# Kernel tuning notes

Hardware: AMD Instinct MI355X
Metric: run time of the kernel (lower is better)

## Reference

```python
import jax, jax.numpy as jnp
import numpy as np
jax.config.update("jax_enable_x64", True)

SR = 44100
STATE_SIZE = 4096
RG0, R10, C10, C20 = 1.0e6, 4.7e5, 3.3e-9, 1.0e-9

# Reconstructed DK-method incidence matrices (3 circuit nodes, 1 vsrc):
#   Vin at node1; C1 node1->node2; R1 node2->gnd; pot top node2->node3;
#   pot bottom node3->gnd; C2 node3->gnd; output at node3 (pot wiper).
_Nu = np.array([[1., 0., 0.]])
_Nx = np.array([[1., -1., 0.], [0., 0., 1.]])
_Nr = np.array([[0., 1., 0.]])
_Nv = np.array([[0., 1., -1.], [0., 0., 1.]])
_No = np.array([[0., 0., 1.]])


def _preamp_forward(x, cond, state, alpha_rg, alpha_r1, alpha_c1, alpha_c2, cond_w, cond_b):
    f64 = jnp.float64
    T = 1.0 / SR
    Nu, Nx, Nr, Nv, No = (jnp.asarray(m, f64) for m in (_Nu, _Nx, _Nr, _Nv, _No))
    Zm = jnp.eye(2, dtype=f64)
    n_nodes, n_vsrc = 3, 1
    zpad = jnp.zeros((2, n_vsrc), f64)
    Nvp = jnp.concatenate([Nv, zpad], axis=1)                      # [2,4]
    Nxp = jnp.concatenate([Nx, zpad], axis=1)                      # [2,4]
    Nop = jnp.concatenate([No, jnp.zeros((1, n_vsrc), f64)], 1)    # [1,4]
    Nup = jnp.concatenate([jnp.zeros((n_nodes, n_vsrc), f64), jnp.eye(n_vsrc, dtype=f64)], 0)  # [4,1]

    # component updates (sigmoid-trimmed around nominal values)
    RG = (0.9 + jax.nn.sigmoid(alpha_rg[0]).astype(f64) * 0.2) * RG0
    R1 = (0.99 + jax.nn.sigmoid(alpha_r1[0]).astype(f64) * 0.02) * R10
    C1 = (0.9 + jax.nn.sigmoid(alpha_c1[0]).astype(f64) * 0.2) * C10
    C2 = (0.9 + jax.nn.sigmoid(alpha_c2[0]).astype(f64) * 0.2) * C20
    Gr = jnp.reshape(1.0 / R1, (1, 1))
    Gx = jnp.diag(jnp.stack([2.0 * C1 / T, 2.0 * C2 / T]))

    # cond block: affine -> sigmoid -> log pot taper
    pot = jax.nn.sigmoid(cond[:, 0] * cond_w[0] + cond_b[0])
    p = jnp.clip((jnp.power(10.0, pot) - 1.0) / 9.0, 1e-4, 1.0 - 1e-4).astype(f64)  # [B]

    # state-space update
    top = jnp.concatenate([Nr.T @ Gr @ Nr + Nx.T @ Gx @ Nx, Nu.T], axis=1)
    bot = jnp.concatenate([Nu, jnp.zeros((n_vsrc, n_vsrc), f64)], axis=1)
    So_inv = jnp.linalg.inv(jnp.concatenate([top, bot], axis=0))   # [4,4]
    Q = Nvp @ So_inv @ Nvp.T                                        # [2,2]
    Ux = Nxp @ So_inv @ Nvp.T                                       # [2,2]
    Uo = Nop @ So_inv @ Nvp.T                                       # [1,2]
    Uu = Nup.T @ So_inv @ Nvp.T                                     # [1,2]
    ZGx = 2.0 * Zm @ Gx
    Ao = ZGx @ Nxp @ So_inv @ Nxp.T - Zm
    Bo = ZGx @ Nxp @ So_inv @ Nup
    Do = Nop @ So_inv @ Nxp.T
    Eo = Nop @ So_inv @ Nup

    d = jnp.stack([(1.0 - p) * RG, p * RG], axis=-1)                # [B,2]
    Rv = d[:, :, None] * jnp.eye(2, dtype=f64)                      # [B,2,2] diag
    RvQ = jnp.linalg.inv(Rv + Q)                                    # [B,2,2]

    ZGxUx = ZGx @ Ux
    A = Ao - ZGxUx @ RvQ @ Ux.T                                     # [B,2,2]
    Bm = Bo - ZGxUx @ RvQ @ Uu.T                                    # [B,2,1]
    Dm = Do - Uo @ RvQ @ Ux.T                                       # [B,1,2]
    Em = Eo - Uo @ RvQ @ Uu.T                                       # [B,1,1]

    # quadratic characteristic poly [1, -tr, det] (= real part of prod(z-eig))
    def poly2(M):
        tr = M[..., 0, 0] + M[..., 1, 1]
        det = M[..., 0, 0] * M[..., 1, 1] - M[..., 0, 1] * M[..., 1, 0]
        return jnp.stack([jnp.ones_like(tr), -tr, det], axis=-1)    # [B,3]

    den = poly2(A)
    num = poly2(A - Bm @ Dm) + (Em[:, 0] - 1.0) * den

    nb = 1 + STATE_SIZE // 2
    z = jnp.exp(-1j * jnp.linspace(0.0, jnp.pi, nb))                # complex128 [nb]

    def polyval(c):  # Horner, highest degree first
        c = c.astype(jnp.complex128)
        return (c[:, 0, None] * z + c[:, 1, None]) * z + c[:, 2, None]  # [B,nb]

    h = polyval(num) / polyval(den)                                 # [B,nb]

    L = x.shape[1]
    st = jnp.concatenate([state[:, L:, :], x], axis=1).astype(f64)  # [B,S,1]
    sf = jnp.fft.rfft(st, axis=1)                                   # [B,nb,1]
    out = jnp.fft.irfft(sf * h[:, :, None], axis=1).astype(jnp.float32)
    return out[:, -L:, :]


def setup_inputs() -> dict:
    key = jax.random.key(0)
    k0, k1, k2 = jax.random.split(key, 3)
    B, L = 2048, 2048
    return {
        "x": jax.random.normal(k0, (B, L, 1), dtype=jnp.float32),
        "cond": jax.random.uniform(k1, (B, 1), dtype=jnp.float32),
        "state": jax.random.normal(k2, (B, STATE_SIZE, 1), dtype=jnp.float32) * 0.1,
        "alpha_rg": jnp.zeros((1,), jnp.float32),
        "alpha_r1": jnp.zeros((1,), jnp.float32),
        "alpha_c1": jnp.zeros((1,), jnp.float32),
        "alpha_c2": jnp.zeros((1,), jnp.float32),
        "cond_w": jnp.ones((1,), jnp.float32),
        "cond_b": jnp.zeros((1,), jnp.float32),
    }


def reference(x, cond, state, alpha_rg, alpha_r1, alpha_c1, alpha_c2, cond_w, cond_b):
    return _preamp_forward(x, cond, state, alpha_rg, alpha_r1, alpha_c1, alpha_c2, cond_w, cond_b)
```

## Files before the change

### kernel.cpp

```cpp
#include <hip/hip_runtime.h>
#include <math.h>

#define NFFT 4096
#define HALF 2048
#define LSEG 2048
#define SSZ 4096

typedef float v2f __attribute__((ext_vector_type(2)));
typedef float v4f __attribute__((ext_vector_type(4)));

static __device__ __forceinline__ v2f cmul(v2f a, v2f b) {
    v2f r;
    asm("v_pk_mul_f32 %0, %1, %2 op_sel:[0,0] op_sel_hi:[0,1]\n\t"
        "v_pk_fma_f32 %0, %1, %2, %0 op_sel:[1,1,0] op_sel_hi:[1,0,1] neg_lo:[1,0,0]"
        : "=&v"(r) : "v"(a), "v"(b));
    return r;
}

static __device__ __forceinline__ v2f cadd_mi(v2f c, v2f d) {
    v2f r;
    asm("v_pk_add_f32 %0, %1, %2 op_sel:[0,1] op_sel_hi:[1,0] neg_hi:[0,1]"
        : "=v"(r) : "v"(c), "v"(d));
    return r;
}

static __device__ __forceinline__ v2f cadd_pi(v2f c, v2f d) {
    v2f r;
    asm("v_pk_add_f32 %0, %1, %2 op_sel:[0,1] op_sel_hi:[1,0] neg_lo:[0,1]"
        : "=v"(r) : "v"(c), "v"(d));
    return r;
}

static __device__ __forceinline__ int PAD(int i) { return i + (i >> 4); }

template <int SGN>
static __device__ __forceinline__ void dft16(v2f r[16]) {
    v2f t[16];
#pragma unroll
    for (int n1 = 0; n1 < 4; ++n1) {
        v2f a = r[n1], b = r[n1 + 4], c = r[n1 + 8], d = r[n1 + 12];
        v2f A = a + c, B = b + d, C = a - c, D = b - d;
        t[n1 * 4 + 0] = A + B;
        t[n1 * 4 + 2] = A - B;
        if (SGN < 0) {
            t[n1 * 4 + 1] = cadd_mi(C, D);
            t[n1 * 4 + 3] = cadd_pi(C, D);
        } else {
            t[n1 * 4 + 1] = cadd_pi(C, D);
            t[n1 * 4 + 3] = cadd_mi(C, D);
        }
    }
    const float CC[10] = {1.f, 0.92387953251f, 0.70710678119f, 0.38268343236f, 0.f,
                          -0.38268343236f, -0.70710678119f, -0.92387953251f, -1.f, -0.92387953251f};
    const float SS[10] = {0.f, 0.38268343236f, 0.70710678119f, 0.92387953251f, 1.f,
                          0.92387953251f, 0.70710678119f, 0.38268343236f, 0.f, -0.38268343236f};
    const float S = (float)SGN;
#pragma unroll
    for (int n1 = 1; n1 < 4; ++n1) {
#pragma unroll
        for (int m2 = 1; m2 < 4; ++m2) {
            const int k = n1 * m2;
            t[n1 * 4 + m2] = cmul(t[n1 * 4 + m2], (v2f){CC[k], S * SS[k]});
        }
    }
#pragma unroll
    for (int m2 = 0; m2 < 4; ++m2) {
        v2f a = t[m2], b = t[4 + m2], c = t[8 + m2], d = t[12 + m2];
        v2f A = a + c, B = b + d, C = a - c, D = b - d;
        r[m2]     = A + B;
        r[m2 + 8] = A - B;
        if (SGN < 0) {
            r[m2 + 4]  = cadd_mi(C, D);
            r[m2 + 12] = cadd_pi(C, D);
        } else {
            r[m2 + 4]  = cadd_pi(C, D);
            r[m2 + 12] = cadd_mi(C, D);
        }
    }
}

static __device__ __forceinline__ void twiddle_chain(v2f r[16], v2f w1) {
    v2f w2 = cmul(w1, w1);
    v2f w3 = cmul(w2, w1);
    v2f w4 = cmul(w2, w2);
    v2f w5 = cmul(w4, w1);
    v2f w6 = cmul(w4, w2);
    v2f w7 = cmul(w4, w3);
    v2f w8 = cmul(w4, w4);
    r[1] = cmul(r[1], w1);   r[2] = cmul(r[2], w2);
    r[3] = cmul(r[3], w3);   r[4] = cmul(r[4], w4);
    r[5] = cmul(r[5], w5);   r[6] = cmul(r[6], w6);
    r[7] = cmul(r[7], w7);   r[8] = cmul(r[8], w8);
    r[9]  = cmul(r[9],  cmul(w8, w1));
    r[10] = cmul(r[10], cmul(w8, w2));
    r[11] = cmul(r[11], cmul(w8, w3));
    r[12] = cmul(r[12], cmul(w8, w4));
    r[13] = cmul(r[13], cmul(w8, w5));
    r[14] = cmul(r[14], cmul(w8, w6));
    r[15] = cmul(r[15], cmul(w8, w7));
}

__global__ __launch_bounds__(256, 4)
void preamp_fft_kernel(const float* __restrict__ x,
                       const float* __restrict__ state,
                       const float* __restrict__ cond,
                       const float* __restrict__ a_rg,
                       const float* __restrict__ a_r1,
                       const float* __restrict__ a_c1,
                       const float* __restrict__ a_c2,
                       const float* __restrict__ cond_w,
                       const float* __restrict__ cond_b,
                       float* __restrict__ out, int B) {
    __shared__ v2f a_s[NFFT + NFFT / 16];
    __shared__ float cf[10];

    const int t = threadIdx.x;
    const int b0 = 2 * blockIdx.x;
    const int b1 = (b0 + 1 < B) ? b0 + 1 : b0;

    const float* st0 = state + (size_t)b0 * SSZ + (SSZ - LSEG);
    const float* xb0 = x + (size_t)b0 * LSEG;
    const float* st1 = state + (size_t)b1 * SSZ + (SSZ - LSEG);
    const float* xb1 = x + (size_t)b1 * LSEG;

#pragma unroll
    for (int q = 0; q < 4; ++q) {
        const int i0 = (t + 256 * q) << 2;
        v4f fa, fb;
        if (q < 2) {
            fa = *(const v4f*)(st0 + i0);
            fb = *(const v4f*)(st1 + i0);
        } else {
            fa = *(const v4f*)(xb0 + (i0 - LSEG));
            fb = *(const v4f*)(xb1 + (i0 - LSEG));
        }
        const int p = PAD(i0);
        a_s[p + 0] = (v2f){fa.x, fb.x};
        a_s[p + 1] = (v2f){fa.y, fb.y};
        a_s[p + 2] = (v2f){fa.z, fb.z};
        a_s[p + 3] = (v2f){fa.w, fb.w};
    }

    if ((t & 127) == 0) {
        const int who = t >> 7;
        const int bb = who ? b1 : b0;

        const double RG = (0.9 + (double)(1.0f / (1.0f + expf(-a_rg[0]))) * 0.2) * 1.0e6;
        const double R1 = (0.99 + (double)(1.0f / (1.0f + expf(-a_r1[0]))) * 0.02) * 4.7e5;
        const double C1 = (0.9 + (double)(1.0f / (1.0f + expf(-a_c1[0]))) * 0.2) * 3.3e-9;
        const double C2 = (0.9 + (double)(1.0f / (1.0f + expf(-a_c2[0]))) * 0.2) * 1.0e-9;
        const double g1 = 1.0 / R1;
        const double gc1 = 2.0 * C1 * 44100.0;
        const double gc2 = 2.0 * C2 * 44100.0;

        float zf = cond[bb] * cond_w[0] + cond_b[0];
        float pot = 1.0f / (1.0f + expf(-zf));
        float prf = (powf(10.0f, pot) - 1.0f) / 9.0f;
        prf = fminf(fmaxf(prf, 1e-4f), 1.0f - 1e-4f);
        const double p = (double)prf;

        const double ds = gc1 + g1;
        double S[4][4] = {
            {0.0, 0.0,        0.0,       1.0},
            {0.0, 1.0 / ds,   0.0,       gc1 / ds},
            {0.0, 0.0,        1.0 / gc2, 0.0},
            {1.0, gc1 / ds,   0.0,       -gc1 * g1 / ds}};

        double Q00 = S[1][1] - S[1][2] - S[2][1] + S[2][2];
        double Q01 = S[1][2] - S[2][2];
        double Q10 = S[2][1] - S[2][2];
        double Q11 = S[2][2];

        double Ux00 = S[0][1] - S[0][2] - S[1][1] + S[1][2];
        double Ux01 = S[0][2] - S[1][2];
        double Ux10 = S[2][1] - S[2][2];
        double Ux11 = S[2][2];

        double Uo0 = S[2][1] - S[2][2], Uo1 = S[2][2];
        double Uu0 = S[3][1] - S[3][2], Uu1 = S[3][2];

        double P00 = S[0][0] - S[0][1] - S[1][0] + S[1][1];
        double P01 = S[0][2] - S[1][2];
        double P10 = S[2][0] - S[2][1];
        double P11 = S[2][2];

        double Ao00 = 2.0 * gc1 * P00 - 1.0, Ao01 = 2.0 * gc1 * P01;
        double Ao10 = 2.0 * gc2 * P10,       Ao11 = 2.0 * gc2 * P11 - 1.0;

        double Bo0 = 2.0 * gc1 * (S[0][3] - S[1][3]);
        double Bo1 = 2.0 * gc2 * S[2][3];

        double Do0 = S[2][0] - S[2][1], Do1 = S[2][2];
        double Eo  = S[2][3];

        double T00 = 2.0 * gc1 * Ux00, T01 = 2.0 * gc1 * Ux01;
        double T10 = 2.0 * gc2 * Ux10, T11 = 2.0 * gc2 * Ux11;

        double d0 = (1.0 - p) * RG, d1v = p * RG;
        double M00 = d0 + Q00, M01 = Q01, M10 = Q10, M11 = d1v + Q11;
        double idet = 1.0 / (M00 * M11 - M01 * M10);
        double G00 =  M11 * idet, G01 = -M01 * idet;
        double G10 = -M10 * idet, G11 =  M00 * idet;

        double TG00 = T00 * G00 + T01 * G10, TG01 = T00 * G01 + T01 * G11;
        double TG10 = T10 * G00 + T11 * G10, TG11 = T10 * G01 + T11 * G11;

        double A00 = Ao00 - (TG00 * Ux00 + TG01 * Ux01);
        double A01 = Ao01 - (TG00 * Ux10 + TG01 * Ux11);
        double A10 = Ao10 - (TG10 * Ux00 + TG11 * Ux01);
        double A11 = Ao11 - (TG10 * Ux10 + TG11 * Ux11);

        double Bm0 = Bo0 - (TG00 * Uu0 + TG01 * Uu1);
        double Bm1 = Bo1 - (TG10 * Uu0 + TG11 * Uu1);

        double w0v = Uo0 * G00 + Uo1 * G10, w1v = Uo0 * G01 + Uo1 * G11;
        double Dm0 = Do0 - (w0v * Ux00 + w1v * Ux01);
        double Dm1 = Do1 - (w0v * Ux10 + w1v * Ux11);
        double Em  = Eo  - (w0v * Uu0 + w1v * Uu1);

        double den1 = -(A00 + A11);
        double den2 = A00 * A11 - A01 * A10;
        double Mm00 = A00 - Bm0 * Dm0, Mm01 = A01 - Bm0 * Dm1;
        double Mm10 = A10 - Bm1 * Dm0, Mm11 = A11 - Bm1 * Dm1;
        double num0 = Em;
        double num1 = -(Mm00 + Mm11) + (Em - 1.0) * den1;
        double num2 = (Mm00 * Mm11 - Mm01 * Mm10) + (Em - 1.0) * den2;

        cf[who * 5 + 0] = (float)num0;
        cf[who * 5 + 1] = (float)num1;
        cf[who * 5 + 2] = (float)(num0 + num1 + num2);
        cf[who * 5 + 3] = (float)den1;
        cf[who * 5 + 4] = (float)(1.0 + den1 + den2);
    }
    __syncthreads();

    const float TW4096 = 0.00153398078788564f;
    const float TW256  = 0.02454369260617026f;
    const float HW4096 = 0.00076699039394282f;

    float swA, cwA;
    __sincosf((float)t * TW4096, &swA, &cwA);
    const int subB = t >> 4, jB = t & 15;
    float swB, cwB;
    __sincosf((float)jB * TW256, &swB, &cwB);

    v2f r[16];

#pragma unroll
    for (int m = 0; m < 16; ++m) r[m] = a_s[PAD(t + 256 * m)];
    dft16<-1>(r);
    twiddle_chain(r, (v2f){cwA, -swA});
#pragma unroll
    for (int m = 0; m < 16; ++m) a_s[PAD(t + 256 * m)] = r[m];
    __syncthreads();

    {
        const int base = subB * 256 + jB;
#pragma unroll
        for (int m = 0; m < 16; ++m) r[m] = a_s[PAD(base + 16 * m)];
        dft16<-1>(r);
        twiddle_chain(r, (v2f){cwB, -swB});
#pragma unroll
        for (int m = 0; m < 16; ++m) a_s[PAD(base + 16 * m)] = r[m];
    }
    __syncthreads();

    {
        const int base = 16 * t;
#pragma unroll
        for (int m = 0; m < 16; ++m) r[m] = a_s[PAD(base + m)];
        dft16<-1>(r);
        const int klo = ((t & 15) << 4) | (t >> 4);
        __syncthreads();
#pragma unroll
        for (int m = 0; m < 16; ++m) a_s[PAD((m << 8) | klo)] = r[m];
    }
    __syncthreads();

    {
        const v2f n0p = {0.5f * cf[0], 0.5f * cf[5]};
        const v2f n1p = {0.5f * cf[1], 0.5f * cf[6]};
        const v2f snp = {0.5f * cf[2], 0.5f * cf[7]};
        const v2f d1p = {cf[3], cf[8]};
        const v2f sdp = {cf[4], cf[9]};

        for (int j = 0; j < 8; ++j) {
            const int k  = t + 256 * j;
            const int kr = (NFFT - k) & (NFFT - 1);
            v2f Wk = a_s[PAD(k)];
            v2f Wr = a_s[PAD(kr)];
            float Xar = Wk.x + Wr.x, Xai = Wk.y - Wr.y;
            float Xbr = Wk.y + Wr.y, Xbi = Wr.x - Wk.x;
            float sh, ch;
            __sincosf((float)k * HW4096, &sh, &ch);
            float m2s = -2.0f * sh;
            float ur = m2s * sh, ui = m2s * ch, pr = ur + 2.0f;
            v2f urp = {ur, ur}, uip = {ui, ui}, prp = {pr, pr};

            v2f tr = n0p * prp + n1p;
            v2f ti = n0p * uip;
            v2f nr = snp + urp * tr - uip * ti;
            v2f ni = urp * ti + uip * tr;
            v2f tb = prp + d1p;
            v2f dr = sdp + urp * tb - uip * uip;
            v2f di = urp * uip + uip * tb;
            v2f mg = dr * dr + di * di;
            v2f iv = { __builtin_amdgcn_rcpf(mg.x), __builtin_amdgcn_rcpf(mg.y) };
            v2f Hr = (nr * dr + ni * di) * iv;
            v2f Hi = (ni * dr - nr * di) * iv;

            float Yar = Hr.x * Xar - Hi.x * Xai, Yai = Hr.x * Xai + Hi.x * Xar;
            float Ybr = Hr.y * Xbr - Hi.y * Xbi, Ybi = Hr.y * Xbi + Hi.y * Xbr;
            a_s[PAD(k)]  = (v2f){Yar - Ybi, Yai + Ybr};
            a_s[PAD(kr)] = (v2f){Yar + Ybi, Ybr - Yai};
        }
        if (t == 0) {
            v2f Wn = a_s[PAD(2048)];
            float Ha = (snp.x - 2.0f * n1p.x) / (sdp.x - 2.0f * d1p.x);
            float Hb = (snp.y - 2.0f * n1p.y) / (sdp.y - 2.0f * d1p.y);
            a_s[PAD(2048)] = (v2f){Ha * (2.0f * Wn.x), Hb * (2.0f * Wn.y)};
        }
    }
    __syncthreads();

    {
        const int base = 16 * t;
        const int klo = ((t & 15) << 4) | (t >> 4);
#pragma unroll
        for (int m = 0; m < 16; ++m) r[m] = a_s[PAD((m << 8) | klo)];
        dft16<1>(r);
        __syncthreads();
#pragma unroll
        for (int m = 0; m < 16; ++m) a_s[PAD(base + m)] = r[m];
    }
    __syncthreads();

    {
        const int base = subB * 256 + jB;
#pragma unroll
        for (int m = 0; m < 16; ++m) r[m] = a_s[PAD(base + 16 * m)];
        twiddle_chain(r, (v2f){cwB, swB});
        dft16<1>(r);
#pragma unroll
        for (int m = 0; m < 16; ++m) a_s[PAD(base + 16 * m)] = r[m];
    }
    __syncthreads();

    {
#pragma unroll
        for (int m = 0; m < 16; ++m) r[m] = a_s[PAD(t + 256 * m)];
        twiddle_chain(r, (v2f){cwA, swA});
        dft16<1>(r);
        const float scale = 1.0f / (float)NFFT;
        float* ob0 = out + (size_t)b0 * LSEG;
        float* ob1 = out + (size_t)b1 * LSEG;
#pragma unroll
        for (int m = 8; m < 16; ++m) {
            const int idx = t + 256 * (m - 8);
            float ya = r[m].x * scale;
            float yb = (b1 != b0) ? r[m].y * scale : ya;
            ob0[idx] = ya;
            ob1[idx] = yb;
        }
    }
}

extern "C" void kernel_launch(void* const* d_in, const int* in_sizes, int n_in,
                              void* d_out, int out_size, void* d_ws, size_t ws_size,
                              hipStream_t stream) {
    const float* x     = (const float*)d_in[0];
    const float* cond  = (const float*)d_in[1];
    const float* state = (const float*)d_in[2];
    const float* a_rg  = (const float*)d_in[3];
    const float* a_r1  = (const float*)d_in[4];
    const float* a_c1  = (const float*)d_in[5];
    const float* a_c2  = (const float*)d_in[6];
    const float* c_w   = (const float*)d_in[7];
    const float* c_b   = (const float*)d_in[8];
    float* out = (float*)d_out;

    const int B = in_sizes[1];

    preamp_fft_kernel<<<dim3((B + 1) / 2), dim3(256), 0, stream>>>(
        x, state, cond, a_rg, a_r1, a_c1, a_c2, c_w, c_b, out, B);
}
```

Measured before the change: 113.0 us.

## Switch FFT to radix-8 with 512 threads and split coefficient computation into prepass

Rewrites the 4096-point FFT from three radix-16 passes over 256 threads to four radix-8 passes over 512 threads, which lowers register pressure per thread and raises the thread count per block. The per-batch double-precision filter coefficient computation moves out of the FFT kernel into a separate small kernel that writes to workspace, so the FFT kernel no longer stalls on one serial thread. The cost is an extra launch, a global round-trip for the coefficients, and more shared-memory passes and barriers.

```diff
diff --git a/kernel.cpp b/kernel.cpp
--- a/kernel.cpp
+++ b/kernel.cpp
@@ -16,14 +16,12 @@
         : "=&v"(r) : "v"(a), "v"(b));
     return r;
 }
-
 static __device__ __forceinline__ v2f cadd_mi(v2f c, v2f d) {
     v2f r;
     asm("v_pk_add_f32 %0, %1, %2 op_sel:[0,1] op_sel_hi:[1,0] neg_hi:[0,1]"
         : "=v"(r) : "v"(c), "v"(d));
     return r;
 }
-
 static __device__ __forceinline__ v2f cadd_pi(v2f c, v2f d) {
     v2f r;
     asm("v_pk_add_f32 %0, %1, %2 op_sel:[0,1] op_sel_hi:[1,0] neg_lo:[0,1]"
@@ -34,85 +32,147 @@
 static __device__ __forceinline__ int PAD(int i) { return i + (i >> 4); }
 
 template <int SGN>
-static __device__ __forceinline__ void dft16(v2f r[16]) {
-    v2f t[16];
-#pragma unroll
-    for (int n1 = 0; n1 < 4; ++n1) {
-        v2f a = r[n1], b = r[n1 + 4], c = r[n1 + 8], d = r[n1 + 12];
-        v2f A = a + c, B = b + d, C = a - c, D = b - d;
-        t[n1 * 4 + 0] = A + B;
-        t[n1 * 4 + 2] = A - B;
-        if (SGN < 0) {
-            t[n1 * 4 + 1] = cadd_mi(C, D);
-            t[n1 * 4 + 3] = cadd_pi(C, D);
-        } else {
-            t[n1 * 4 + 1] = cadd_pi(C, D);
-            t[n1 * 4 + 3] = cadd_mi(C, D);
-        }
-    }
-    const float CC[10] = {1.f, 0.92387953251f, 0.70710678119f, 0.38268343236f, 0.f,
-                          -0.38268343236f, -0.70710678119f, -0.92387953251f, -1.f, -0.92387953251f};
-    const float SS[10] = {0.f, 0.38268343236f, 0.70710678119f, 0.92387953251f, 1.f,
-                          0.92387953251f, 0.70710678119f, 0.38268343236f, 0.f, -0.38268343236f};
+static __device__ __forceinline__ void dft8(v2f r[8]) {
+    v2f A0 = r[0] + r[4], C0 = r[0] - r[4];
+    v2f B0 = r[2] + r[6], D0 = r[2] - r[6];
+    v2f E0 = A0 + B0, E2 = A0 - B0;
+    v2f E1 = (SGN < 0) ? cadd_mi(C0, D0) : cadd_pi(C0, D0);
+    v2f E3 = (SGN < 0) ? cadd_pi(C0, D0) : cadd_mi(C0, D0);
+    v2f A1 = r[1] + r[5], C1 = r[1] - r[5];
+    v2f B1 = r[3] + r[7], D1 = r[3] - r[7];
+    v2f O0 = A1 + B1, O2 = A1 - B1;
+    v2f O1 = (SGN < 0) ? cadd_mi(C1, D1) : cadd_pi(C1, D1);
+    v2f O3 = (SGN < 0) ? cadd_pi(C1, D1) : cadd_mi(C1, D1);
+    const float HQ = 0.70710678118654752f;
     const float S = (float)SGN;
-#pragma unroll
-    for (int n1 = 1; n1 < 4; ++n1) {
-#pragma unroll
-        for (int m2 = 1; m2 < 4; ++m2) {
-            const int k = n1 * m2;
-            t[n1 * 4 + m2] = cmul(t[n1 * 4 + m2], (v2f){CC[k], S * SS[k]});
-        }
-    }
-#pragma unroll
-    for (int m2 = 0; m2 < 4; ++m2) {
-        v2f a = t[m2], b = t[4 + m2], c = t[8 + m2], d = t[12 + m2];
-        v2f A = a + c, B = b + d, C = a - c, D = b - d;
-        r[m2]     = A + B;
-        r[m2 + 8] = A - B;
-        if (SGN < 0) {
-            r[m2 + 4]  = cadd_mi(C, D);
-            r[m2 + 12] = cadd_pi(C, D);
-        } else {
-            r[m2 + 4]  = cadd_pi(C, D);
-            r[m2 + 12] = cadd_mi(C, D);
-        }
-    }
-}
-
-static __device__ __forceinline__ void twiddle_chain(v2f r[16], v2f w1) {
+    v2f T1 = cmul(O1, (v2f){HQ, S * HQ});
+    v2f T3 = cmul(O3, (v2f){-HQ, S * HQ});
+    r[0] = E0 + O0;  r[4] = E0 - O0;
+    r[1] = E1 + T1;  r[5] = E1 - T1;
+    r[2] = (SGN < 0) ? cadd_mi(E2, O2) : cadd_pi(E2, O2);
+    r[6] = (SGN < 0) ? cadd_pi(E2, O2) : cadd_mi(E2, O2);
+    r[3] = E3 + T3;  r[7] = E3 - T3;
+}
+
+static __device__ __forceinline__ void twiddle8(v2f r[8], v2f w1) {
     v2f w2 = cmul(w1, w1);
     v2f w3 = cmul(w2, w1);
     v2f w4 = cmul(w2, w2);
     v2f w5 = cmul(w4, w1);
-    v2f w6 = cmul(w4, w2);
+    v2f w6 = cmul(w3, w3);
     v2f w7 = cmul(w4, w3);
-    v2f w8 = cmul(w4, w4);
-    r[1] = cmul(r[1], w1);   r[2] = cmul(r[2], w2);
-    r[3] = cmul(r[3], w3);   r[4] = cmul(r[4], w4);
-    r[5] = cmul(r[5], w5);   r[6] = cmul(r[6], w6);
-    r[7] = cmul(r[7], w7);   r[8] = cmul(r[8], w8);
-    r[9]  = cmul(r[9],  cmul(w8, w1));
-    r[10] = cmul(r[10], cmul(w8, w2));
-    r[11] = cmul(r[11], cmul(w8, w3));
-    r[12] = cmul(r[12], cmul(w8, w4));
-    r[13] = cmul(r[13], cmul(w8, w5));
-    r[14] = cmul(r[14], cmul(w8, w6));
-    r[15] = cmul(r[15], cmul(w8, w7));
-}
-
-__global__ __launch_bounds__(256, 4)
+    r[1] = cmul(r[1], w1); r[2] = cmul(r[2], w2); r[3] = cmul(r[3], w3);
+    r[4] = cmul(r[4], w4); r[5] = cmul(r[5], w5); r[6] = cmul(r[6], w6);
+    r[7] = cmul(r[7], w7);
+}
+
+__global__ __launch_bounds__(256)
+void preamp_coef_kernel(const float* __restrict__ cond,
+                        const float* __restrict__ a_rg,
+                        const float* __restrict__ a_r1,
+                        const float* __restrict__ a_c1,
+                        const float* __restrict__ a_c2,
+                        const float* __restrict__ cond_w,
+                        const float* __restrict__ cond_b,
+                        float* __restrict__ cf_g, int B) {
+    const int bb = blockIdx.x * 256 + threadIdx.x;
+    if (bb >= B) return;
+
+    const double RG = (0.9 + (double)(1.0f / (1.0f + expf(-a_rg[0]))) * 0.2) * 1.0e6;
+    const double R1 = (0.99 + (double)(1.0f / (1.0f + expf(-a_r1[0]))) * 0.02) * 4.7e5;
+    const double C1 = (0.9 + (double)(1.0f / (1.0f + expf(-a_c1[0]))) * 0.2) * 3.3e-9;
+    const double C2 = (0.9 + (double)(1.0f / (1.0f + expf(-a_c2[0]))) * 0.2) * 1.0e-9;
+    const double g1 = 1.0 / R1;
+    const double gc1 = 2.0 * C1 * 44100.0;
+    const double gc2 = 2.0 * C2 * 44100.0;
+
+    float zf = cond[bb] * cond_w[0] + cond_b[0];
+    float pot = 1.0f / (1.0f + expf(-zf));
+    float prf = (powf(10.0f, pot) - 1.0f) / 9.0f;
+    prf = fminf(fmaxf(prf, 1e-4f), 1.0f - 1e-4f);
+    const double p = (double)prf;
+
+    const double ds = gc1 + g1;
+    double S[4][4] = {
+        {0.0, 0.0,        0.0,       1.0},
+        {0.0, 1.0 / ds,   0.0,       gc1 / ds},
+        {0.0, 0.0,        1.0 / gc2, 0.0},
+        {1.0, gc1 / ds,   0.0,       -gc1 * g1 / ds}};
+
+    double Q00 = S[1][1] - S[1][2] - S[2][1] + S[2][2];
+    double Q01 = S[1][2] - S[2][2];
+    double Q10 = S[2][1] - S[2][2];
+    double Q11 = S[2][2];
+
+    double Ux00 = S[0][1] - S[0][2] - S[1][1] + S[1][2];
+    double Ux01 = S[0][2] - S[1][2];
+    double Ux10 = S[2][1] - S[2][2];
+    double Ux11 = S[2][2];
+
+    double Uo0 = S[2][1] - S[2][2], Uo1 = S[2][2];
+    double Uu0 = S[3][1] - S[3][2], Uu1 = S[3][2];
+
+    double P00 = S[0][0] - S[0][1] - S[1][0] + S[1][1];
+    double P01 = S[0][2] - S[1][2];
+    double P10 = S[2][0] - S[2][1];
+    double P11 = S[2][2];
+
+    double Ao00 = 2.0 * gc1 * P00 - 1.0, Ao01 = 2.0 * gc1 * P01;
+    double Ao10 = 2.0 * gc2 * P10,       Ao11 = 2.0 * gc2 * P11 - 1.0;
+
+    double Bo0 = 2.0 * gc1 * (S[0][3] - S[1][3]);
+    double Bo1 = 2.0 * gc2 * S[2][3];
+
+    double Do0 = S[2][0] - S[2][1], Do1 = S[2][2];
+    double Eo  = S[2][3];
+
+    double T00 = 2.0 * gc1 * Ux00, T01 = 2.0 * gc1 * Ux01;
+    double T10 = 2.0 * gc2 * Ux10, T11 = 2.0 * gc2 * Ux11;
+
+    double d0 = (1.0 - p) * RG, d1v = p * RG;
+    double M00 = d0 + Q00, M01 = Q01, M10 = Q10, M11 = d1v + Q11;
+    double idet = 1.0 / (M00 * M11 - M01 * M10);
+    double G00 =  M11 * idet, G01 = -M01 * idet;
+    double G10 = -M10 * idet, G11 =  M00 * idet;
+
+    double TG00 = T00 * G00 + T01 * G10, TG01 = T00 * G01 + T01 * G11;
+    double TG10 = T10 * G00 + T11 * G10, TG11 = T10 * G01 + T11 * G11;
+
+    double A00 = Ao00 - (TG00 * Ux00 + TG01 * Ux01);
+    double A01 = Ao01 - (TG00 * Ux10 + TG01 * Ux11);
+    double A10 = Ao10 - (TG10 * Ux00 + TG11 * Ux01);
+    double A11 = Ao11 - (TG10 * Ux10 + TG11 * Ux11);
+
+    double Bm0 = Bo0 - (TG00 * Uu0 + TG01 * Uu1);
+    double Bm1 = Bo1 - (TG10 * Uu0 + TG11 * Uu1);
+
+    double w0v = Uo0 * G00 + Uo1 * G10, w1v = Uo0 * G01 + Uo1 * G11;
+    double Dm0 = Do0 - (w0v * Ux00 + w1v * Ux01);
+    double Dm1 = Do1 - (w0v * Ux10 + w1v * Ux11);
+    double Em  = Eo  - (w0v * Uu0 + w1v * Uu1);
+
+    double den1 = -(A00 + A11);
+    double den2 = A00 * A11 - A01 * A10;
+    double Mm00 = A00 - Bm0 * Dm0, Mm01 = A01 - Bm0 * Dm1;
+    double Mm10 = A10 - Bm1 * Dm0, Mm11 = A11 - Bm1 * Dm1;
+    double num0 = Em;
+    double num1 = -(Mm00 + Mm11) + (Em - 1.0) * den1;
+    double num2 = (Mm00 * Mm11 - Mm01 * Mm10) + (Em - 1.0) * den2;
+
+    float* o = cf_g + (size_t)bb * 5;
+    o[0] = (float)(0.5 * num0);
+    o[1] = (float)(0.5 * num1);
+    o[2] = (float)(0.5 * (num0 + num1 + num2));
+    o[3] = (float)den1;
+    o[4] = (float)(1.0 + den1 + den2);
+}
+
+__global__ __launch_bounds__(512, 8)
 void preamp_fft_kernel(const float* __restrict__ x,
                        const float* __restrict__ state,
-                       const float* __restrict__ cond,
-                       const float* __restrict__ a_rg,
-                       const float* __restrict__ a_r1,
-                       const float* __restrict__ a_c1,
-                       const float* __restrict__ a_c2,
-                       const float* __restrict__ cond_w,
-                       const float* __restrict__ cond_b,
+                       const float* __restrict__ cf_g,
                        float* __restrict__ out, int B) {
     __shared__ v2f a_s[NFFT + NFFT / 16];
-    __shared__ float cf[10];
 
     const int t = threadIdx.x;
     const int b0 = 2 * blockIdx.x;
@@ -124,168 +184,87 @@
     const float* xb1 = x + (size_t)b1 * LSEG;
 
 #pragma unroll
-    for (int q = 0; q < 4; ++q) {
-        const int i0 = (t + 256 * q) << 2;
+    for (int q = 0; q < 2; ++q) {
+        const int i0 = (t + 512 * q) << 2;
         v4f fa, fb;
-        if (q < 2) {
+        if (q == 0) {
             fa = *(const v4f*)(st0 + i0);
             fb = *(const v4f*)(st1 + i0);
         } else {
             fa = *(const v4f*)(xb0 + (i0 - LSEG));
             fb = *(const v4f*)(xb1 + (i0 - LSEG));
         }
-        const int p = PAD(i0);
-        a_s[p + 0] = (v2f){fa.x, fb.x};
-        a_s[p + 1] = (v2f){fa.y, fb.y};
-        a_s[p + 2] = (v2f){fa.z, fb.z};
-        a_s[p + 3] = (v2f){fa.w, fb.w};
+        const int pp = PAD(i0);
+        a_s[pp + 0] = (v2f){fa.x, fb.x};
+        a_s[pp + 1] = (v2f){fa.y, fb.y};
+        a_s[pp + 2] = (v2f){fa.z, fb.z};
+        a_s[pp + 3] = (v2f){fa.w, fb.w};
     }
-
-    if ((t & 127) == 0) {
-        const int who = t >> 7;
-        const int bb = who ? b1 : b0;
-
-        const double RG = (0.9 + (double)(1.0f / (1.0f + expf(-a_rg[0]))) * 0.2) * 1.0e6;
-        const double R1 = (0.99 + (double)(1.0f / (1.0f + expf(-a_r1[0]))) * 0.02) * 4.7e5;
-        const double C1 = (0.9 + (double)(1.0f / (1.0f + expf(-a_c1[0]))) * 0.2) * 3.3e-9;
-        const double C2 = (0.9 + (double)(1.0f / (1.0f + expf(-a_c2[0]))) * 0.2) * 1.0e-9;
-        const double g1 = 1.0 / R1;
-        const double gc1 = 2.0 * C1 * 44100.0;
-        const double gc2 = 2.0 * C2 * 44100.0;
-
-        float zf = cond[bb] * cond_w[0] + cond_b[0];
-        float pot = 1.0f / (1.0f + expf(-zf));
-        float prf = (powf(10.0f, pot) - 1.0f) / 9.0f;
-        prf = fminf(fmaxf(prf, 1e-4f), 1.0f - 1e-4f);
-        const double p = (double)prf;
-
-        const double ds = gc1 + g1;
-        double S[4][4] = {
-            {0.0, 0.0,        0.0,       1.0},
-            {0.0, 1.0 / ds,   0.0,       gc1 / ds},
-            {0.0, 0.0,        1.0 / gc2, 0.0},
-            {1.0, gc1 / ds,   0.0,       -gc1 * g1 / ds}};
-
-        double Q00 = S[1][1] - S[1][2] - S[2][1] + S[2][2];
-        double Q01 = S[1][2] - S[2][2];
-        double Q10 = S[2][1] - S[2][2];
-        double Q11 = S[2][2];
-
-        double Ux00 = S[0][1] - S[0][2] - S[1][1] + S[1][2];
-        double Ux01 = S[0][2] - S[1][2];
-        double Ux10 = S[2][1] - S[2][2];
-        double Ux11 = S[2][2];
-
-        double Uo0 = S[2][1] - S[2][2], Uo1 = S[2][2];
-        double Uu0 = S[3][1] - S[3][2], Uu1 = S[3][2];
-
-        double P00 = S[0][0] - S[0][1] - S[1][0] + S[1][1];
-        double P01 = S[0][2] - S[1][2];
-        double P10 = S[2][0] - S[2][1];
-        double P11 = S[2][2];
-
-        double Ao00 = 2.0 * gc1 * P00 - 1.0, Ao01 = 2.0 * gc1 * P01;
-        double Ao10 = 2.0 * gc2 * P10,       Ao11 = 2.0 * gc2 * P11 - 1.0;
-
-        double Bo0 = 2.0 * gc1 * (S[0][3] - S[1][3]);
-        double Bo1 = 2.0 * gc2 * S[2][3];
-
-        double Do0 = S[2][0] - S[2][1], Do1 = S[2][2];
-        double Eo  = S[2][3];
-
-        double T00 = 2.0 * gc1 * Ux00, T01 = 2.0 * gc1 * Ux01;
-        double T10 = 2.0 * gc2 * Ux10, T11 = 2.0 * gc2 * Ux11;
-
-        double d0 = (1.0 - p) * RG, d1v = p * RG;
-        double M00 = d0 + Q00, M01 = Q01, M10 = Q10, M11 = d1v + Q11;
-        double idet = 1.0 / (M00 * M11 - M01 * M10);
-        double G00 =  M11 * idet, G01 = -M01 * idet;
-        double G10 = -M10 * idet, G11 =  M00 * idet;
-
-        double TG00 = T00 * G00 + T01 * G10, TG01 = T00 * G01 + T01 * G11;
-        double TG10 = T10 * G00 + T11 * G10, TG11 = T10 * G01 + T11 * G11;
-
-        double A00 = Ao00 - (TG00 * Ux00 + TG01 * Ux01);
-        double A01 = Ao01 - (TG00 * Ux10 + TG01 * Ux11);
-        double A10 = Ao10 - (TG10 * Ux00 + TG11 * Ux01);
-        double A11 = Ao11 - (TG10 * Ux10 + TG11 * Ux11);
-
-        double Bm0 = Bo0 - (TG00 * Uu0 + TG01 * Uu1);
-        double Bm1 = Bo1 - (TG10 * Uu0 + TG11 * Uu1);
-
-        double w0v = Uo0 * G00 + Uo1 * G10, w1v = Uo0 * G01 + Uo1 * G11;
-        double Dm0 = Do0 - (w0v * Ux00 + w1v * Ux01);
-        double Dm1 = Do1 - (w0v * Ux10 + w1v * Ux11);
-        double Em  = Eo  - (w0v * Uu0 + w1v * Uu1);
-
-        double den1 = -(A00 + A11);
-        double den2 = A00 * A11 - A01 * A10;
-        double Mm00 = A00 - Bm0 * Dm0, Mm01 = A01 - Bm0 * Dm1;
-        double Mm10 = A10 - Bm1 * Dm0, Mm11 = A11 - Bm1 * Dm1;
-        double num0 = Em;
-        double num1 = -(Mm00 + Mm11) + (Em - 1.0) * den1;
-        double num2 = (Mm00 * Mm11 - Mm01 * Mm10) + (Em - 1.0) * den2;
-
-        cf[who * 5 + 0] = (float)num0;
-        cf[who * 5 + 1] = (float)num1;
-        cf[who * 5 + 2] = (float)(num0 + num1 + num2);
-        cf[who * 5 + 3] = (float)den1;
-        cf[who * 5 + 4] = (float)(1.0 + den1 + den2);
-    }
     __syncthreads();
 
     const float TW4096 = 0.00153398078788564f;
-    const float TW256  = 0.02454369260617026f;
+    const float TW512  = 0.01227184630308513f;
+    const float TW64   = 0.09817477042468103f;
     const float HW4096 = 0.00076699039394282f;
 
     float swA, cwA;
     __sincosf((float)t * TW4096, &swA, &cwA);
-    const int subB = t >> 4, jB = t & 15;
+    const int j2 = t & 63, sub2 = t >> 6;
     float swB, cwB;
-    __sincosf((float)jB * TW256, &swB, &cwB);
-
-    v2f r[16];
-
-#pragma unroll
-    for (int m = 0; m < 16; ++m) r[m] = a_s[PAD(t + 256 * m)];
-    dft16<-1>(r);
-    twiddle_chain(r, (v2f){cwA, -swA});
-#pragma unroll
-    for (int m = 0; m < 16; ++m) a_s[PAD(t + 256 * m)] = r[m];
+    __sincosf((float)j2 * TW512, &swB, &cwB);
+    const int j3 = t & 7, sub3 = t >> 3;
+    float swC, cwC;
+    __sincosf((float)j3 * TW64, &swC, &cwC);
+
+    const int base2 = sub2 * 512 + j2;
+    const int base3 = sub3 * 64 + j3;
+    const int klo = ((t & 7) << 6) | (((t >> 3) & 7) << 3) | (t >> 6);
+
+    v2f r[8];
+
+#pragma unroll
+    for (int m = 0; m < 8; ++m) r[m] = a_s[PAD(t + 512 * m)];
+    dft8<-1>(r);
+    twiddle8(r, (v2f){cwA, -swA});
+#pragma unroll
+    for (int m = 0; m < 8; ++m) a_s[PAD(t + 512 * m)] = r[m];
+    __syncthreads();
+
+#pragma unroll
+    for (int m = 0; m < 8; ++m) r[m] = a_s[PAD(base2 + 64 * m)];
+    dft8<-1>(r);
+    twiddle8(r, (v2f){cwB, -swB});
+#pragma unroll
+    for (int m = 0; m < 8; ++m) a_s[PAD(base2 + 64 * m)] = r[m];
+    __syncthreads();
+
+#pragma unroll
+    for (int m = 0; m < 8; ++m) r[m] = a_s[PAD(base3 + 8 * m)];
+    dft8<-1>(r);
+    twiddle8(r, (v2f){cwC, -swC});
+#pragma unroll
+    for (int m = 0; m < 8; ++m) a_s[PAD(base3 + 8 * m)] = r[m];
+    __syncthreads();
+
+#pragma unroll
+    for (int m = 0; m < 8; ++m) r[m] = a_s[PAD(8 * t + m)];
+    dft8<-1>(r);
+    __syncthreads();
+#pragma unroll
+    for (int m = 0; m < 8; ++m) a_s[PAD((m << 9) | klo)] = r[m];
     __syncthreads();
 
     {
-        const int base = subB * 256 + jB;
-#pragma unroll
-        for (int m = 0; m < 16; ++m) r[m] = a_s[PAD(base + 16 * m)];
-        dft16<-1>(r);
-        twiddle_chain(r, (v2f){cwB, -swB});
-#pragma unroll
-        for (int m = 0; m < 16; ++m) a_s[PAD(base + 16 * m)] = r[m];
-    }
-    __syncthreads();
-
-    {
-        const int base = 16 * t;
-#pragma unroll
-        for (int m = 0; m < 16; ++m) r[m] = a_s[PAD(base + m)];
-        dft16<-1>(r);
-        const int klo = ((t & 15) << 4) | (t >> 4);
-        __syncthreads();
-#pragma unroll
-        for (int m = 0; m < 16; ++m) a_s[PAD((m << 8) | klo)] = r[m];
-    }
-    __syncthreads();
-
-    {
-        const v2f n0p = {0.5f * cf[0], 0.5f * cf[5]};
-        const v2f n1p = {0.5f * cf[1], 0.5f * cf[6]};
-        const v2f snp = {0.5f * cf[2], 0.5f * cf[7]};
-        const v2f d1p = {cf[3], cf[8]};
-        const v2f sdp = {cf[4], cf[9]};
-
-        for (int j = 0; j < 8; ++j) {
-            const int k  = t + 256 * j;
+        const float* cA = cf_g + (size_t)b0 * 5;
+        const float* cB = cf_g + (size_t)b1 * 5;
+        const v2f n0p = {cA[0], cB[0]};
+        const v2f n1p = {cA[1], cB[1]};
+        const v2f snp = {cA[2], cB[2]};
+        const v2f d1p = {cA[3], cB[3]};
+        const v2f sdp = {cA[4], cB[4]};
+
+        for (int j = 0; j < 4; ++j) {
+            const int k  = t + 512 * j;
             const int kr = (NFFT - k) & (NFFT - 1);
             v2f Wk = a_s[PAD(k)];
             v2f Wr = a_s[PAD(kr)];
@@ -323,40 +302,41 @@
     }
     __syncthreads();
 
+#pragma unroll
+    for (int m = 0; m < 8; ++m) r[m] = a_s[PAD((m << 9) | klo)];
+    dft8<1>(r);
+    __syncthreads();
+#pragma unroll
+    for (int m = 0; m < 8; ++m) a_s[PAD(8 * t + m)] = r[m];
+    __syncthreads();
+
+#pragma unroll
+    for (int m = 0; m < 8; ++m) r[m] = a_s[PAD(base3 + 8 * m)];
+    twiddle8(r, (v2f){cwC, swC});
+    dft8<1>(r);
+#pragma unroll
+    for (int m = 0; m < 8; ++m) a_s[PAD(base3 + 8 * m)] = r[m];
+    __syncthreads();
+
+#pragma unroll
+    for (int m = 0; m < 8; ++m) r[m] = a_s[PAD(base2 + 64 * m)];
+    twiddle8(r, (v2f){cwB, swB});
+    dft8<1>(r);
+#pragma unroll
+    for (int m = 0; m < 8; ++m) a_s[PAD(base2 + 64 * m)] = r[m];
+    __syncthreads();
+
+#pragma unroll
+    for (int m = 0; m < 8; ++m) r[m] = a_s[PAD(t + 512 * m)];
+    twiddle8(r, (v2f){cwA, swA});
+    dft8<1>(r);
     {
-        const int base = 16 * t;
-        const int klo = ((t & 15) << 4) | (t >> 4);
-#pragma unroll
-        for (int m = 0; m < 16; ++m) r[m] = a_s[PAD((m << 8) | klo)];
-        dft16<1>(r);
-        __syncthreads();
-#pragma unroll
-        for (int m = 0; m < 16; ++m) a_s[PAD(base + m)] = r[m];
-    }
-    __syncthreads();
-
-    {
-        const int base = subB * 256 + jB;
-#pragma unroll
-        for (int m = 0; m < 16; ++m) r[m] = a_s[PAD(base + 16 * m)];
-        twiddle_chain(r, (v2f){cwB, swB});
-        dft16<1>(r);
-#pragma unroll
-        for (int m = 0; m < 16; ++m) a_s[PAD(base + 16 * m)] = r[m];
-    }
-    __syncthreads();
-
-    {
-#pragma unroll
-        for (int m = 0; m < 16; ++m) r[m] = a_s[PAD(t + 256 * m)];
-        twiddle_chain(r, (v2f){cwA, swA});
-        dft16<1>(r);
         const float scale = 1.0f / (float)NFFT;
         float* ob0 = out + (size_t)b0 * LSEG;
         float* ob1 = out + (size_t)b1 * LSEG;
 #pragma unroll
-        for (int m = 8; m < 16; ++m) {
-            const int idx = t + 256 * (m - 8);
+        for (int m = 4; m < 8; ++m) {
+            const int idx = t + 512 * (m - 4);
             float ya = r[m].x * scale;
             float yb = (b1 != b0) ? r[m].y * scale : ya;
             ob0[idx] = ya;
@@ -380,7 +360,10 @@
     float* out = (float*)d_out;
 
     const int B = in_sizes[1];
-
-    preamp_fft_kernel<<<dim3((B + 1) / 2), dim3(256), 0, stream>>>(
-        x, state, cond, a_rg, a_r1, a_c1, a_c2, c_w, c_b, out, B);
-}
+    float* cf_ws = (float*)d_ws;
+
+    preamp_coef_kernel<<<dim3((B + 255) / 256), dim3(256), 0, stream>>>(
+        cond, a_rg, a_r1, a_c1, a_c2, c_w, c_b, cf_ws, B);
+    preamp_fft_kernel<<<dim3((B + 1) / 2), dim3(512), 0, stream>>>(
+        x, state, cf_ws, out, B);
+}
```

After: 116.9 us. 1.03x slower.
